# Kernel optimization log

Hardware: AMD Instinct MI355X
Metric: run time of the kernel (lower is better)

## Reference

```python
import jax, jax.numpy as jnp
import numpy as np

L, D = 2048, 1024
D_INNER = 2 * D          # expand=2
D_STATE = 16
D_CONV = 4
DT_RANK = D // 16        # ceil(1024/16) = 64
HID = 4 * D
EPS = 1e-5


def _layernorm(x, g, b):
    mu = jnp.mean(x, axis=-1, keepdims=True)
    var = jnp.mean(jnp.square(x - mu), axis=-1, keepdims=True)
    return (x - mu) * jax.lax.rsqrt(var + EPS) * g + b


def setup_inputs() -> dict:
    key = jax.random.key(0)
    ks = jax.random.split(key, 12)
    f = lambda k, sh, s=0.02: (jax.random.normal(k, sh, jnp.float32) * s)
    return {
        "x": jax.random.normal(ks[0], (L, D), jnp.float32),
        "ln1_g": jnp.ones((D,), jnp.float32),
        "ln1_b": jnp.zeros((D,), jnp.float32),
        "ln2_g": jnp.ones((D,), jnp.float32),
        "ln2_b": jnp.zeros((D,), jnp.float32),
        "in_proj_w": f(ks[1], (2 * D_INNER, D)),
        "conv_w": f(ks[2], (D_INNER, D_CONV), 0.1),
        "conv_b": jnp.zeros((D_INNER,), jnp.float32),
        "x_proj_w": f(ks[3], (DT_RANK + 2 * D_STATE, D_INNER)),
        "dt_proj_w": f(ks[4], (D_INNER, DT_RANK), 0.1),
        "dt_proj_b": f(ks[5], (D_INNER,), 0.1),
        "A_log": jnp.log(jnp.broadcast_to(
            jnp.arange(1, D_STATE + 1, dtype=jnp.float32), (D_INNER, D_STATE))),
        "D_param": jnp.ones((D_INNER,), jnp.float32),
        "out_proj_w": f(ks[6], (D, D_INNER)),
        "ffn_w1": f(ks[7], (HID, D)),
        "ffn_b1": jnp.zeros((HID,), jnp.float32),
        "ffn_w2": f(ks[8], (D, HID)),
        "ffn_b2": jnp.zeros((D,), jnp.float32),
    }


def _mamba(x, in_proj_w, conv_w, conv_b, x_proj_w, dt_proj_w, dt_proj_b,
           A_log, D_param, out_proj_w):
    # x: (L, D)
    xz = x @ in_proj_w.T                    # (L, 2*d_inner)
    xm, z = xz[:, :D_INNER], xz[:, D_INNER:]
    # causal depthwise conv1d, kernel d_conv, output length L
    xp = jnp.pad(xm, ((D_CONV - 1, 0), (0, 0)))
    xc = conv_b
    for k in range(D_CONV):                 # 4 taps, fixed small loop
        xc = xc + xp[k:k + L] * conv_w[None, :, k]
    xc = jax.nn.silu(xc)                    # (L, d_inner)
    proj = xc @ x_proj_w.T                  # (L, dt_rank + 2*d_state)
    dt = proj[:, :DT_RANK]
    B = proj[:, DT_RANK:DT_RANK + D_STATE]  # (L, d_state)
    C = proj[:, DT_RANK + D_STATE:]         # (L, d_state)
    delta = jax.nn.softplus(dt @ dt_proj_w.T + dt_proj_b)  # (L, d_inner)
    A = -jnp.exp(A_log)                     # (d_inner, d_state)
    dA = jnp.exp(delta[:, :, None] * A[None])               # (L, d_inner, d_state)
    dBx = delta[:, :, None] * B[:, None, :] * xc[:, :, None]

    def step(h, inp):
        dA_t, dBx_t, C_t = inp
        h = h * dA_t + dBx_t                # (d_inner, d_state)
        y = jnp.einsum('ds,s->d', h, C_t)
        return h, y

    h0 = jnp.zeros((D_INNER, D_STATE), x.dtype)
    _, ys = jax.lax.scan(step, h0, (dA, dBx, C))            # ys: (L, d_inner)
    y = ys + xc * D_param
    y = y * jax.nn.silu(z)
    return y @ out_proj_w.T                 # (L, D)


def reference(x, ln1_g, ln1_b, ln2_g, ln2_b, in_proj_w, conv_w, conv_b,
              x_proj_w, dt_proj_w, dt_proj_b, A_log, D_param, out_proj_w,
              ffn_w1, ffn_b1, ffn_w2, ffn_b2):
    residual = x
    h = _layernorm(x, ln1_g, ln1_b)
    h = _mamba(h, in_proj_w, conv_w, conv_b, x_proj_w, dt_proj_w, dt_proj_b,
               A_log, D_param, out_proj_w)
    h = h + residual
    # FFN has an internal residual around the normed input, plus outer residual
    n = _layernorm(h, ln2_g, ln2_b)
    f = n + (jax.nn.relu(n @ ffn_w1.T + ffn_b1) @ ffn_w2.T + ffn_b2)
    return h + f
```

## Files before the change

kernel.cpp:

```cpp
#include <hip/hip_runtime.h>
#include <hip/hip_bf16.h>
#include <math.h>

#define L_SEQ 2048
#define DMODEL 1024
#define DINNER 2048
#define DSTATE 16
#define DTRANK 64
#define NHID 4096
#define NC 64
#define LC 32

typedef __bf16 bf16_t;
typedef __bf16 bf16x4 __attribute__((ext_vector_type(4)));
typedef __bf16 bf16x8 __attribute__((ext_vector_type(8)));
typedef float f32x4 __attribute__((ext_vector_type(4)));

__device__ __forceinline__ void async_cp16(const bf16_t* g, bf16_t* l) {
    __builtin_amdgcn_global_load_lds(
        (const __attribute__((address_space(1))) void*)g,
        (__attribute__((address_space(3))) void*)l, 16, 0, 0);
}

template <int EPI, int OUTBF16>
__global__ __launch_bounds__(256) void gemm_async(
    const bf16_t* __restrict__ A, int lda,
    const bf16_t* __restrict__ W, int ldw,
    void* __restrict__ Cv, int ldc,
    int N, int Kslice, long cstride,
    const float* __restrict__ bias)
{
    __shared__ bf16_t As[128 * 32];
    __shared__ bf16_t Ws[128 * 32];

    const int tid  = threadIdx.x;
    const int lane = tid & 63;
    const int w    = tid >> 6;
    const int m0   = blockIdx.y * 128;
    const int n0   = blockIdx.x * 128;
    const int kz   = blockIdx.z;
    const int k0   = kz * Kslice;

    const int p   = lane & 3;
    const int r0  = 2 * w * 16 + (lane >> 2);
    const int r1  = r0 + 16;
    const int dc0 = (p - ((r0 >> 1) & 3)) & 3;
    const int dc1 = (p - ((r1 >> 1) & 3)) & 3;

    const bf16_t* gA0 = A + (size_t)(m0 + r0) * lda + k0 + dc0 * 8;
    const bf16_t* gA1 = A + (size_t)(m0 + r1) * lda + k0 + dc1 * 8;
    int gn0 = n0 + r0; if (gn0 > N - 1) gn0 = N - 1;
    int gn1 = n0 + r1; if (gn1 > N - 1) gn1 = N - 1;
    const bf16_t* gW0 = W + (size_t)gn0 * ldw + k0 + dc0 * 8;
    const bf16_t* gW1 = W + (size_t)gn1 * ldw + k0 + dc1 * 8;
    bf16_t* lA0 = &As[(2 * w) * 512];
    bf16_t* lA1 = &As[(2 * w) * 512 + 512];
    bf16_t* lW0 = &Ws[(2 * w) * 512];
    bf16_t* lW1 = &Ws[(2 * w) * 512 + 512];

    const int wr   = w >> 1;
    const int wc   = w & 1;
    const int quad = lane >> 4;
    const int lr   = lane & 15;
    int offA[4], offW[4];
    #pragma unroll
    for (int i = 0; i < 4; ++i) {
        int ra = wr * 64 + i * 16 + lr;
        offA[i] = ra * 32 + (((quad + ((ra >> 1) & 3)) & 3) * 8);
        int rb = wc * 64 + i * 16 + lr;
        offW[i] = rb * 32 + (((quad + ((rb >> 1) & 3)) & 3) * 8);
    }

    f32x4 acc[4][4] = {};
    const int niter = Kslice >> 5;
    for (int it = 0; it < niter; ++it) {
        async_cp16(gA0, lA0);
        async_cp16(gA1, lA1);
        async_cp16(gW0, lW0);
        async_cp16(gW1, lW1);
        gA0 += 32; gA1 += 32; gW0 += 32; gW1 += 32;
        __builtin_amdgcn_s_waitcnt(0);
        __syncthreads();

        bf16x8 af[4], bw[4];
        #pragma unroll
        for (int i = 0; i < 4; ++i) af[i] = *(const bf16x8*)&As[offA[i]];
        #pragma unroll
        for (int j = 0; j < 4; ++j) bw[j] = *(const bf16x8*)&Ws[offW[j]];
        #pragma unroll
        for (int i = 0; i < 4; ++i)
            #pragma unroll
            for (int j = 0; j < 4; ++j)
                acc[i][j] = __builtin_amdgcn_mfma_f32_16x16x32_bf16(af[i], bw[j], acc[i][j], 0, 0, 0);
        __syncthreads();
    }

    float* Cf   = (float*)Cv + (size_t)kz * cstride;
    bf16_t* Cb  = (bf16_t*)Cv;
    #pragma unroll
    for (int i = 0; i < 4; ++i) {
        int row0 = m0 + wr * 64 + i * 16 + quad * 4;
        #pragma unroll
        for (int j = 0; j < 4; ++j) {
            int col = n0 + wc * 64 + j * 16 + lr;
            if (col < N) {
                float bv = (EPI == 2 || EPI == 3) ? bias[col] : 0.f;
                #pragma unroll
                for (int r = 0; r < 4; ++r) {
                    float v = acc[i][j][r];
                    if (EPI == 2) v = fmaxf(v + bv, 0.f);
                    else if (EPI == 3) {
                        float t = v + bv;
                        v = fmaxf(t, 0.f) + log1pf(__expf(-fabsf(t)));
                    }
                    size_t o = (size_t)(row0 + r) * ldc + col;
                    if (OUTBF16) Cb[o] = (bf16_t)v;
                    else         Cf[o] = v;
                }
            }
        }
    }
}

__global__ __launch_bounds__(256) void cvt_weights(
    const float* __restrict__ s0, const float* __restrict__ s1,
    const float* __restrict__ s2, const float* __restrict__ s3,
    const float* __restrict__ s4, const float* __restrict__ s5,
    bf16_t* __restrict__ dst)
{
    int e = (blockIdx.x * 256 + threadIdx.x) * 4;
    const float* src; int local;
    if      (e < 4194304)  { src = s0; local = e; }
    else if (e < 4390912)  { src = s1; local = e - 4194304; }
    else if (e < 4521984)  { src = s2; local = e - 4390912; }
    else if (e < 6619136)  { src = s3; local = e - 4521984; }
    else if (e < 10813440) { src = s4; local = e - 6619136; }
    else                   { src = s5; local = e - 10813440; }
    float4 v = *(const float4*)(src + local);
    bf16x4 o;
    o[0] = (bf16_t)v.x; o[1] = (bf16_t)v.y; o[2] = (bf16_t)v.z; o[3] = (bf16_t)v.w;
    *(bf16x4*)(dst + e) = o;
}

template <int MODE>
__global__ __launch_bounds__(256) void ln_kernel(
    const float* __restrict__ x, const float* __restrict__ g,
    const float* __restrict__ b, float* __restrict__ outf,
    bf16_t* __restrict__ outb)
{
    const int row = blockIdx.x;
    const float* xr = x + (size_t)row * DMODEL;
    float v[4];
    float s = 0.f, sq = 0.f;
    #pragma unroll
    for (int i = 0; i < 4; ++i) {
        v[i] = xr[threadIdx.x + i * 256];
        s += v[i]; sq += v[i] * v[i];
    }
    #pragma unroll
    for (int off = 32; off > 0; off >>= 1) {
        s += __shfl_xor(s, off); sq += __shfl_xor(sq, off);
    }
    __shared__ float rs_[4], rq_[4];
    int w = threadIdx.x >> 6;
    if ((threadIdx.x & 63) == 0) { rs_[w] = s; rq_[w] = sq; }
    __syncthreads();
    s  = rs_[0] + rs_[1] + rs_[2] + rs_[3];
    sq = rq_[0] + rq_[1] + rq_[2] + rq_[3];
    float mu  = s * (1.f / DMODEL);
    float var = sq * (1.f / DMODEL) - mu * mu;
    float rsd = rsqrtf(var + 1e-5f);
    #pragma unroll
    for (int i = 0; i < 4; ++i) {
        int col = threadIdx.x + i * 256;
        float o = (v[i] - mu) * rsd * g[col] + b[col];
        if (MODE == 1) outf[(size_t)row * DMODEL + col] = o;
        outb[(size_t)row * DMODEL + col] = (bf16_t)o;
    }
}

__global__ __launch_bounds__(256) void conv_silu(
    const bf16_t* __restrict__ xz, const float* __restrict__ cw,
    const float* __restrict__ cb, bf16_t* __restrict__ xc)
{
    int gid = blockIdx.x * 256 + threadIdx.x;
    int c = gid & (DINNER - 1);
    int t = gid >> 11;
    float acc = cb[c];
    #pragma unroll
    for (int k = 0; k < 4; ++k) {
        int tt = t + k - 3;
        if (tt >= 0) acc += (float)xz[(size_t)tt * (2 * DINNER) + c] * cw[c * 4 + k];
    }
    float sig = 1.f / (1.f + __expf(-acc));
    xc[gid] = (bf16_t)(acc * sig);
}

__global__ __launch_bounds__(256) void scan_pass1(
    const float* __restrict__ delta, const bf16_t* __restrict__ xc,
    const float* __restrict__ proj, const float* __restrict__ A_log,
    float* __restrict__ carryH, float* __restrict__ sumd)
{
    const int c = blockIdx.x;
    const int d = blockIdx.y * 256 + threadIdx.x;
    const int t0 = c * LC;

    __shared__ float Bs[LC][DSTATE];
    for (int i = threadIdx.x; i < LC * DSTATE; i += 256) {
        int tt = i >> 4, s = i & 15;
        Bs[tt][s] = proj[(size_t)(t0 + tt) * 96 + DTRANK + s];
    }
    __syncthreads();

    float a[DSTATE], h[DSTATE];
    #pragma unroll
    for (int s = 0; s < DSTATE; ++s) {
        a[s] = -__expf(A_log[d * DSTATE + s]);
        h[s] = 0.f;
    }
    float sd = 0.f;
    for (int i = 0; i < LC; ++i) {
        int t = t0 + i;
        float dl = delta[(size_t)t * DINNER + d];
        float x  = (float)xc[(size_t)t * DINNER + d];
        sd += dl;
        float dx = dl * x;
        #pragma unroll
        for (int s = 0; s < DSTATE; ++s)
            h[s] = h[s] * __expf(dl * a[s]) + dx * Bs[i][s];
    }
    #pragma unroll
    for (int s = 0; s < DSTATE; ++s)
        carryH[((size_t)c * DINNER + d) * DSTATE + s] = h[s];
    sumd[c * DINNER + d] = sd;
}

__global__ __launch_bounds__(256) void scan_pass2(
    const float* __restrict__ A_log, const float* __restrict__ carryH,
    const float* __restrict__ sumd, float* __restrict__ hinit)
{
    int idx = blockIdx.x * 256 + threadIdx.x;
    int d = idx >> 4;
    float a = -__expf(A_log[idx]);
    float hc = 0.f;
    for (int c = 0; c < NC; ++c) {
        hinit[(size_t)c * (DINNER * DSTATE) + idx] = hc;
        float P = __expf(a * sumd[c * DINNER + d]);
        hc = carryH[(size_t)c * (DINNER * DSTATE) + idx] + P * hc;
    }
}

__global__ __launch_bounds__(256) void scan_pass3(
    const float* __restrict__ delta, const bf16_t* __restrict__ xc,
    const float* __restrict__ proj, const float* __restrict__ A_log,
    const float* __restrict__ hinit, const float* __restrict__ Dp,
    const bf16_t* __restrict__ xz, bf16_t* __restrict__ yact)
{
    const int c = blockIdx.x;
    const int d = blockIdx.y * 256 + threadIdx.x;
    const int t0 = c * LC;

    __shared__ float Bs[LC][DSTATE], Cs[LC][DSTATE];
    for (int i = threadIdx.x; i < LC * DSTATE; i += 256) {
        int tt = i >> 4, s = i & 15;
        size_t base = (size_t)(t0 + tt) * 96;
        Bs[tt][s] = proj[base + DTRANK + s];
        Cs[tt][s] = proj[base + DTRANK + DSTATE + s];
    }
    __syncthreads();

    float a[DSTATE], h[DSTATE];
    #pragma unroll
    for (int s = 0; s < DSTATE; ++s) {
        a[s] = -__expf(A_log[d * DSTATE + s]);
        h[s] = hinit[(size_t)c * (DINNER * DSTATE) + d * DSTATE + s];
    }
    float DD = Dp[d];
    for (int i = 0; i < LC; ++i) {
        int t = t0 + i;
        float dl = delta[(size_t)t * DINNER + d];
        float x  = (float)xc[(size_t)t * DINNER + d];
        float dx = dl * x;
        float y = 0.f;
        #pragma unroll
        for (int s = 0; s < DSTATE; ++s) {
            h[s] = h[s] * __expf(dl * a[s]) + dx * Bs[i][s];
            y += h[s] * Cs[i][s];
        }
        float yv = y + x * DD;
        float z = (float)xz[(size_t)t * (2 * DINNER) + DINNER + d];
        float sil = z / (1.f + __expf(-z));
        yact[(size_t)t * DINNER + d] = (bf16_t)(yv * sil);
    }
}

__global__ __launch_bounds__(256) void reduce4(
    const float* __restrict__ part, float* __restrict__ proj,
    bf16_t* __restrict__ projdt)
{
    int i = blockIdx.x * 256 + threadIdx.x;
    float v = 0.f;
    #pragma unroll
    for (int s = 0; s < 16; ++s) v += part[(size_t)s * 196608 + i];
    proj[i] = v;
    int row = i / 96;
    int col = i - row * 96;
    if (col < DTRANK) projdt[row * DTRANK + col] = (bf16_t)v;
}

__global__ __launch_bounds__(256) void reduce9(
    const float* __restrict__ part, const float* __restrict__ x,
    float* __restrict__ hres)
{
    int i = (blockIdx.x * 256 + threadIdx.x) * 4;
    float4 a = *(const float4*)(part + i);
    float4 b = *(const float4*)(part + 2097152 + i);
    float4 c = *(const float4*)(x + i);
    float4 o = make_float4(a.x + b.x + c.x, a.y + b.y + c.y,
                           a.z + b.z + c.z, a.w + b.w + c.w);
    *(float4*)(hres + i) = o;
}

__global__ __launch_bounds__(256) void reduce12(
    const float* __restrict__ part, const float* __restrict__ b2,
    const float* __restrict__ hres, const float* __restrict__ nbuf,
    float* __restrict__ out)
{
    int i = (blockIdx.x * 256 + threadIdx.x) * 4;
    float4 a = *(const float4*)(part + i);
    float4 b = *(const float4*)(part + 2097152 + i);
    float4 bb = *(const float4*)(b2 + (i & (DMODEL - 1)));
    float4 h = *(const float4*)(hres + i);
    float4 n = *(const float4*)(nbuf + i);
    float4 o = make_float4(a.x + b.x + bb.x + h.x + n.x,
                           a.y + b.y + bb.y + h.y + n.y,
                           a.z + b.z + bb.z + h.z + n.z,
                           a.w + b.w + bb.w + h.w + n.w);
    *(float4*)(out + i) = o;
}

extern "C" void kernel_launch(void* const* d_in, const int* in_sizes, int n_in,
                              void* d_out, int out_size, void* d_ws, size_t ws_size,
                              hipStream_t stream)
{
    const float* x        = (const float*)d_in[0];
    const float* ln1_g    = (const float*)d_in[1];
    const float* ln1_b    = (const float*)d_in[2];
    const float* ln2_g    = (const float*)d_in[3];
    const float* ln2_b    = (const float*)d_in[4];
    const float* in_proj  = (const float*)d_in[5];
    const float* conv_w   = (const float*)d_in[6];
    const float* conv_b   = (const float*)d_in[7];
    const float* x_proj   = (const float*)d_in[8];
    const float* dt_proj  = (const float*)d_in[9];
    const float* dt_b     = (const float*)d_in[10];
    const float* A_log    = (const float*)d_in[11];
    const float* D_param  = (const float*)d_in[12];
    const float* out_proj = (const float*)d_in[13];
    const float* ffn_w1   = (const float*)d_in[14];
    const float* ffn_b1   = (const float*)d_in[15];
    const float* ffn_w2   = (const float*)d_in[16];
    const float* ffn_b2   = (const float*)d_in[17];
    float* out = (float*)d_out;

    char* base = (char*)d_ws;
    bf16_t* Wb     = (bf16_t*)(base);
    bf16_t* w_inp  = Wb;
    bf16_t* w_xp   = Wb + 4194304;
    bf16_t* w_dtp  = Wb + 4390912;
    bf16_t* w_outp = Wb + 4521984;
    bf16_t* w_f1   = Wb + 6619136;
    bf16_t* w_f2   = Wb + 10813440;

    bf16_t* h1b    = (bf16_t*)(base + 30015488);
    float*  proj   = (float*)(base + 30015488);
    bf16_t* projdt = (bf16_t*)(base + 30015488 + 786432);
    bf16_t* xz     = (bf16_t*)(base + 34209792);
    bf16_t* ffnh   = xz;
    bf16_t* xc     = (bf16_t*)(base + 50987008);
    float*  part   = (float*)(base + 59375616);
    float*  delta  = part;
    float*  carry  = (float*)(base + 76152832);
    bf16_t* nbufb  = (bf16_t*)carry;
    float*  sumd   = (float*)(base + 84541440);
    float*  hinit  = (float*)(base + 85065728);
    float*  nbuf   = hinit;
    bf16_t* yact   = (bf16_t*)(base + 93454336);
    float*  hres   = (float*)(base + 101842944);

    cvt_weights<<<14656, 256, 0, stream>>>(in_proj, x_proj, dt_proj, out_proj,
                                           ffn_w1, ffn_w2, Wb);
    ln_kernel<0><<<L_SEQ, 256, 0, stream>>>(x, ln1_g, ln1_b, nullptr, h1b);
    gemm_async<0, 1><<<dim3(32, 16, 1), 256, 0, stream>>>(
        h1b, DMODEL, w_inp, DMODEL, xz, 4096, 4096, 1024, 0, nullptr);
    conv_silu<<<(L_SEQ * DINNER) / 256, 256, 0, stream>>>(xz, conv_w, conv_b, xc);
    gemm_async<0, 0><<<dim3(1, 16, 16), 256, 0, stream>>>(
        xc, DINNER, w_xp, DINNER, part, 96, 96, 128, 196608L, nullptr);
    reduce4<<<768, 256, 0, stream>>>(part, proj, projdt);
    gemm_async<3, 0><<<dim3(16, 16, 1), 256, 0, stream>>>(
        projdt, DTRANK, w_dtp, DTRANK, delta, DINNER, DINNER, DTRANK, 0, dt_b);
    scan_pass1<<<dim3(NC, DINNER / 256), 256, 0, stream>>>(delta, xc, proj, A_log, carry, sumd);
    scan_pass2<<<(DINNER * DSTATE) / 256, 256, 0, stream>>>(A_log, carry, sumd, hinit);
    scan_pass3<<<dim3(NC, DINNER / 256), 256, 0, stream>>>(delta, xc, proj, A_log, hinit,
                                                           D_param, xz, yact);
    gemm_async<0, 0><<<dim3(8, 16, 2), 256, 0, stream>>>(
        yact, DINNER, w_outp, DINNER, part, DMODEL, DMODEL, 1024, 2097152L, nullptr);
    reduce9<<<2048, 256, 0, stream>>>(part, x, hres);
    ln_kernel<1><<<L_SEQ, 256, 0, stream>>>(hres, ln2_g, ln2_b, nbuf, nbufb);
    gemm_async<2, 1><<<dim3(32, 16, 1), 256, 0, stream>>>(
        nbufb, DMODEL, w_f1, DMODEL, ffnh, NHID, NHID, 1024, 0, ffn_b1);
    gemm_async<0, 0><<<dim3(8, 16, 2), 256, 0, stream>>>(
        ffnh, NHID, w_f2, NHID, part, DMODEL, DMODEL, 2048, 2097152L, nullptr);
    reduce12<<<2048, 256, 0, stream>>>(part, ffn_b2, hres, nbuf, out);
}
```

Measured before the change: 410.3 us.

## Pipeline GEMM loads with 4-stage LDS ring and bf16 split-K partials

The GEMM kernel now keeps a four-buffer LDS ring, prefetching three K-tiles ahead. It uses vmcnt-based partial waits and a single barrier per iteration instead of draining all loads and syncing twice, which lets global loads overlap with MFMA work. The out-proj and FFN2 GEMMs now split K four ways and write bf16 partials, and the reduce kernels sum four bf16 slices, to raise parallelism and cut partial-sum traffic. The costs are 64KB of LDS per block, which limits occupancy, and some precision loss from rounding partials to bf16.

```diff
diff --git a/kernel.cpp b/kernel.cpp
--- a/kernel.cpp
+++ b/kernel.cpp
@@ -16,6 +16,10 @@
 typedef __bf16 bf16x8 __attribute__((ext_vector_type(8)));
 typedef float f32x4 __attribute__((ext_vector_type(4)));
 
+#define WAIT_VM0 0x0F70
+#define WAIT_VM4 0x0F74
+#define WAIT_VM8 0x0F78
+
 __device__ __forceinline__ void async_cp16(const bf16_t* g, bf16_t* l) {
     __builtin_amdgcn_global_load_lds(
         (const __attribute__((address_space(1))) void*)g,
@@ -30,8 +34,8 @@
     int N, int Kslice, long cstride,
     const float* __restrict__ bias)
 {
-    __shared__ bf16_t As[128 * 32];
-    __shared__ bf16_t Ws[128 * 32];
+    __shared__ bf16_t As[4 * 4096];
+    __shared__ bf16_t Ws[4 * 4096];
 
     const int tid  = threadIdx.x;
     const int lane = tid & 63;
@@ -53,10 +57,9 @@
     int gn1 = n0 + r1; if (gn1 > N - 1) gn1 = N - 1;
     const bf16_t* gW0 = W + (size_t)gn0 * ldw + k0 + dc0 * 8;
     const bf16_t* gW1 = W + (size_t)gn1 * ldw + k0 + dc1 * 8;
-    bf16_t* lA0 = &As[(2 * w) * 512];
-    bf16_t* lA1 = &As[(2 * w) * 512 + 512];
-    bf16_t* lW0 = &Ws[(2 * w) * 512];
-    bf16_t* lW1 = &Ws[(2 * w) * 512 + 512];
+
+    const int lo0 = (2 * w) * 512;
+    const int lo1 = lo0 + 512;
 
     const int wr   = w >> 1;
     const int wc   = w & 1;
@@ -71,32 +74,52 @@
         offW[i] = rb * 32 + (((quad + ((rb >> 1) & 3)) & 3) * 8);
     }
 
+    const int niter = Kslice >> 5;
+
+    #pragma unroll
+    for (int j = 0; j < 3; ++j) {
+        if (j < niter) {
+            int sb = j * 4096;
+            async_cp16(gA0, &As[sb + lo0]);
+            async_cp16(gA1, &As[sb + lo1]);
+            async_cp16(gW0, &Ws[sb + lo0]);
+            async_cp16(gW1, &Ws[sb + lo1]);
+            gA0 += 32; gA1 += 32; gW0 += 32; gW1 += 32;
+        }
+    }
+
     f32x4 acc[4][4] = {};
-    const int niter = Kslice >> 5;
     for (int it = 0; it < niter; ++it) {
-        async_cp16(gA0, lA0);
-        async_cp16(gA1, lA1);
-        async_cp16(gW0, lW0);
-        async_cp16(gW1, lW1);
-        gA0 += 32; gA1 += 32; gW0 += 32; gW1 += 32;
-        __builtin_amdgcn_s_waitcnt(0);
-        __syncthreads();
-
+        if (it + 3 <= niter)      __builtin_amdgcn_s_waitcnt(WAIT_VM8);
+        else if (it + 2 <= niter) __builtin_amdgcn_s_waitcnt(WAIT_VM4);
+        else                      __builtin_amdgcn_s_waitcnt(WAIT_VM0);
+        __builtin_amdgcn_s_barrier();
+        asm volatile("" ::: "memory");
+
+        if (it + 3 < niter) {
+            int sb = ((it + 3) & 3) * 4096;
+            async_cp16(gA0, &As[sb + lo0]);
+            async_cp16(gA1, &As[sb + lo1]);
+            async_cp16(gW0, &Ws[sb + lo0]);
+            async_cp16(gW1, &Ws[sb + lo1]);
+            gA0 += 32; gA1 += 32; gW0 += 32; gW1 += 32;
+        }
+
+        const int cb = (it & 3) * 4096;
         bf16x8 af[4], bw[4];
         #pragma unroll
-        for (int i = 0; i < 4; ++i) af[i] = *(const bf16x8*)&As[offA[i]];
-        #pragma unroll
-        for (int j = 0; j < 4; ++j) bw[j] = *(const bf16x8*)&Ws[offW[j]];
+        for (int i = 0; i < 4; ++i) af[i] = *(const bf16x8*)&As[cb + offA[i]];
+        #pragma unroll
+        for (int j = 0; j < 4; ++j) bw[j] = *(const bf16x8*)&Ws[cb + offW[j]];
         #pragma unroll
         for (int i = 0; i < 4; ++i)
             #pragma unroll
             for (int j = 0; j < 4; ++j)
                 acc[i][j] = __builtin_amdgcn_mfma_f32_16x16x32_bf16(af[i], bw[j], acc[i][j], 0, 0, 0);
-        __syncthreads();
-    }
-
-    float* Cf   = (float*)Cv + (size_t)kz * cstride;
-    bf16_t* Cb  = (bf16_t*)Cv;
+    }
+
+    float*  Cf = (float*)Cv + (size_t)kz * cstride;
+    bf16_t* Cb = (bf16_t*)Cv + (size_t)kz * cstride;
     #pragma unroll
     for (int i = 0; i < 4; ++i) {
         int row0 = m0 + wr * 64 + i * 16 + quad * 4;
@@ -309,34 +332,37 @@
 }
 
 __global__ __launch_bounds__(256) void reduce9(
-    const float* __restrict__ part, const float* __restrict__ x,
+    const bf16_t* __restrict__ part, const float* __restrict__ x,
     float* __restrict__ hres)
 {
     int i = (blockIdx.x * 256 + threadIdx.x) * 4;
-    float4 a = *(const float4*)(part + i);
-    float4 b = *(const float4*)(part + 2097152 + i);
     float4 c = *(const float4*)(x + i);
-    float4 o = make_float4(a.x + b.x + c.x, a.y + b.y + c.y,
-                           a.z + b.z + c.z, a.w + b.w + c.w);
-    *(float4*)(hres + i) = o;
+    float s0 = c.x, s1 = c.y, s2 = c.z, s3 = c.w;
+    #pragma unroll
+    for (int sl = 0; sl < 4; ++sl) {
+        bf16x4 v = *(const bf16x4*)(part + (size_t)sl * 2097152 + i);
+        s0 += (float)v[0]; s1 += (float)v[1]; s2 += (float)v[2]; s3 += (float)v[3];
+    }
+    *(float4*)(hres + i) = make_float4(s0, s1, s2, s3);
 }
 
 __global__ __launch_bounds__(256) void reduce12(
-    const float* __restrict__ part, const float* __restrict__ b2,
+    const bf16_t* __restrict__ part, const float* __restrict__ b2,
     const float* __restrict__ hres, const float* __restrict__ nbuf,
     float* __restrict__ out)
 {
     int i = (blockIdx.x * 256 + threadIdx.x) * 4;
-    float4 a = *(const float4*)(part + i);
-    float4 b = *(const float4*)(part + 2097152 + i);
     float4 bb = *(const float4*)(b2 + (i & (DMODEL - 1)));
-    float4 h = *(const float4*)(hres + i);
-    float4 n = *(const float4*)(nbuf + i);
-    float4 o = make_float4(a.x + b.x + bb.x + h.x + n.x,
-                           a.y + b.y + bb.y + h.y + n.y,
-                           a.z + b.z + bb.z + h.z + n.z,
-                           a.w + b.w + bb.w + h.w + n.w);
-    *(float4*)(out + i) = o;
+    float4 h  = *(const float4*)(hres + i);
+    float4 n  = *(const float4*)(nbuf + i);
+    float s0 = bb.x + h.x + n.x, s1 = bb.y + h.y + n.y;
+    float s2 = bb.z + h.z + n.z, s3 = bb.w + h.w + n.w;
+    #pragma unroll
+    for (int sl = 0; sl < 4; ++sl) {
+        bf16x4 v = *(const bf16x4*)(part + (size_t)sl * 2097152 + i);
+        s0 += (float)v[0]; s1 += (float)v[1]; s2 += (float)v[2]; s3 += (float)v[3];
+    }
+    *(float4*)(out + i) = make_float4(s0, s1, s2, s3);
 }
 
 extern "C" void kernel_launch(void* const* d_in, const int* in_sizes, int n_in,
@@ -380,6 +406,7 @@
     bf16_t* xc     = (bf16_t*)(base + 50987008);
     float*  part   = (float*)(base + 59375616);
     float*  delta  = part;
+    bf16_t* partb  = (bf16_t*)part;
     float*  carry  = (float*)(base + 76152832);
     bf16_t* nbufb  = (bf16_t*)carry;
     float*  sumd   = (float*)(base + 84541440);
@@ -403,13 +430,13 @@
     scan_pass2<<<(DINNER * DSTATE) / 256, 256, 0, stream>>>(A_log, carry, sumd, hinit);
     scan_pass3<<<dim3(NC, DINNER / 256), 256, 0, stream>>>(delta, xc, proj, A_log, hinit,
                                                            D_param, xz, yact);
-    gemm_async<0, 0><<<dim3(8, 16, 2), 256, 0, stream>>>(
-        yact, DINNER, w_outp, DINNER, part, DMODEL, DMODEL, 1024, 2097152L, nullptr);
-    reduce9<<<2048, 256, 0, stream>>>(part, x, hres);
+    gemm_async<0, 1><<<dim3(8, 16, 4), 256, 0, stream>>>(
+        yact, DINNER, w_outp, DINNER, partb, DMODEL, DMODEL, 512, 2097152L, nullptr);
+    reduce9<<<2048, 256, 0, stream>>>(partb, x, hres);
     ln_kernel<1><<<L_SEQ, 256, 0, stream>>>(hres, ln2_g, ln2_b, nbuf, nbufb);
     gemm_async<2, 1><<<dim3(32, 16, 1), 256, 0, stream>>>(
         nbufb, DMODEL, w_f1, DMODEL, ffnh, NHID, NHID, 1024, 0, ffn_b1);
-    gemm_async<0, 0><<<dim3(8, 16, 2), 256, 0, stream>>>(
-        ffnh, NHID, w_f2, NHID, part, DMODEL, DMODEL, 2048, 2097152L, nullptr);
-    reduce12<<<2048, 256, 0, stream>>>(part, ffn_b2, hres, nbuf, out);
-}
+    gemm_async<0, 1><<<dim3(8, 16, 4), 256, 0, stream>>>(
+        ffnh, NHID, w_f2, NHID, partb, DMODEL, DMODEL, 1024, 2097152L, nullptr);
+    reduce12<<<2048, 256, 0, stream>>>(partb, ffn_b2, hres, nbuf, out);
+}
```

Result: faster. 379.1 us (-7.6%).
